# Kernel optimization log

Measured on AMD Instinct MI355X. Metric: run time of the kernel, lower is better.

Reference implementation:

```python
import jax, jax.numpy as jnp
import numpy as np

SEQ_LEN = 512
MAX_SPAN = 15
BATCH = 8
HIDDEN = 1024
WIDTH_DIM = 64
NUM_LABELS = 3


def _enumerate_spans(seq_len, max_span):
    starts, ends = [], []
    for s in range(seq_len):
        for e in range(s, min(s + max_span, seq_len)):
            starts.append(s)
            ends.append(e)
    return np.asarray(starts, np.int32), np.asarray(ends, np.int32)


def setup_inputs() -> dict:
    key = jax.random.key(0)
    k = jax.random.split(key, 6)
    starts, ends = _enumerate_spans(SEQ_LEN, MAX_SPAN)  # N = 7575
    d_in = HIDDEN * 2 + WIDTH_DIM  # 2112
    return {
        "sequence_output": jax.random.normal(k[0], (BATCH, SEQ_LEN, HIDDEN), jnp.float32),
        "width_emb": jax.random.normal(k[1], (MAX_SPAN, WIDTH_DIM), jnp.float32) * 0.02,
        "W1": jax.random.normal(k[2], (d_in, HIDDEN), jnp.float32) * (1.0 / np.sqrt(d_in)),
        "b1": jnp.zeros((HIDDEN,), jnp.float32),
        "W2": jax.random.normal(k[3], (HIDDEN, NUM_LABELS), jnp.float32) * (1.0 / np.sqrt(HIDDEN)),
        "b2": jnp.zeros((NUM_LABELS,), jnp.float32),
        "span_starts": jnp.asarray(starts),
        "span_ends": jnp.asarray(ends),
    }


def reference(sequence_output, width_emb, W1, b1, W2, b2, span_starts, span_ends):
    # Gather start/end token representations for every candidate span.
    B = sequence_output.shape[0]
    N = span_starts.shape[0]
    start_repr = sequence_output[:, span_starts]            # [B, N, H]
    end_repr = sequence_output[:, span_ends]                # [B, N, H]
    width_repr = width_emb[span_ends - span_starts]         # [N, 64]
    width_repr = jnp.broadcast_to(width_repr[None], (B, N, width_repr.shape[-1]))
    span_reprs = jnp.concatenate([start_repr, end_repr, width_repr], axis=-1)  # [B, N, 2H+64]
    # Span classifier MLP (dropout is identity in eval mode).
    h = jax.nn.relu(jnp.einsum("bnd,dh->bnh", span_reprs, W1) + b1)
    logits = jnp.einsum("bnh,hl->bnl", h, W2) + b2          # [B, N, num_labels]
    return logits
```

## Files before the change

### kernel.cpp

```cpp
#include <hip/hip_runtime.h>
#include <stdint.h>

#define SEQ 512
#define BATCH 8
#define HID 1024

typedef __attribute__((ext_vector_type(8))) __bf16 bf16x8;
typedef __attribute__((ext_vector_type(4))) float f32x4;

__device__ __forceinline__ unsigned short f2bf(float f) {
    unsigned int u = __float_as_uint(f);
    unsigned int r = 0x7fffu + ((u >> 16) & 1u);
    return (unsigned short)((u + r) >> 16);
}

__device__ __forceinline__ void unpack8(uint4 v, float* f) {
    f[0] = __uint_as_float(v.x << 16);
    f[1] = __uint_as_float(v.x & 0xffff0000u);
    f[2] = __uint_as_float(v.y << 16);
    f[3] = __uint_as_float(v.y & 0xffff0000u);
    f[4] = __uint_as_float(v.z << 16);
    f[5] = __uint_as_float(v.z & 0xffff0000u);
    f[6] = __uint_as_float(v.w << 16);
    f[7] = __uint_as_float(v.w & 0xffff0000u);
}

__global__ __launch_bounds__(256) void k_prep(const float* __restrict__ seq,
                                              const float* __restrict__ wemb,
                                              const float* __restrict__ W1,
                                              const float* __restrict__ b1,
                                              ushort* __restrict__ seqb,
                                              ushort* __restrict__ Bt,
                                              ushort* __restrict__ Rbf) {
    __shared__ float tile[32][33];
    const int bid = blockIdx.x;
    const int tid = threadIdx.x;
    if (bid < 4096) {
        int i = bid * 256 + tid;
        float4 v = ((const float4*)seq)[i];
        ushort4 o;
        o.x = f2bf(v.x); o.y = f2bf(v.y); o.z = f2bf(v.z); o.w = f2bf(v.w);
        ((ushort4*)seqb)[i] = o;
    } else if (bid < 6144) {
        int idx = bid - 4096;
        int nb = (idx & 63) * 32, kb = (idx >> 6) * 32;
        int tx = tid & 31, ty = tid >> 5;
        int n = nb + tx;
        int rb = (n < 1024) ? 0 : 1024;
        int nc = n - rb;
#pragma unroll
        for (int i = 0; i < 4; ++i) {
            int k = kb + ty + i * 8;
            tile[ty + i * 8][tx] = W1[(size_t)(rb + k) * 1024 + nc];
        }
        __syncthreads();
#pragma unroll
        for (int i = 0; i < 4; ++i) {
            int n2 = nb + ty + i * 8;
            Bt[(size_t)n2 * 1024 + kb + tx] = f2bf(tile[tx][ty + i * 8]);
        }
    } else {
        int idx = (bid - 6144) * 256 + tid;
        int w = idx >> 10, j = idx & 1023;
        float acc = b1[j];
#pragma unroll
        for (int c = 0; c < 64; ++c)
            acc = fmaf(wemb[w * 64 + c], W1[(size_t)(2048 + c) * 1024 + j], acc);
        Rbf[idx] = f2bf(acc);
    }
}

__global__ __launch_bounds__(512) void k_gemm(const ushort* __restrict__ A,
                                              const ushort* __restrict__ Bt,
                                              ushort* __restrict__ P,
                                              ushort* __restrict__ Q) {
    __shared__ ushort Al[2][8192];
    __shared__ ushort Bl[2][8192];
    const int tid = threadIdx.x;
    const int wid = tid >> 6;
    const int lane = tid & 63;
    const int bid = blockIdx.x;
    const int swz = ((bid & 7) << 6) | (bid >> 3);
    const int n0 = (swz & 15) * 128;
    const int m0 = (swz >> 4) * 128;
    const int wm = (wid >> 2) * 64;
    const int wn = (wid & 3) * 32;
    const int srow = lane >> 2;
    const int scol = (lane & 3) * 8;
    const int fr = lane & 15;
    const int fk = (lane >> 4) * 8;

    f32x4 acc[4][2] = {};

    const ushort* Abase = A  + (size_t)(m0 + srow) * 1024 + scol;
    const ushort* Bbase = Bt + (size_t)(n0 + srow) * 1024 + scol;

#define STAGE(buf, k0)                                                                     \
    {                                                                                      \
        _Pragma("unroll")                                                                  \
        for (int r = 0; r < 2; ++r) {                                                      \
            int c = wid + 8 * r;                                                           \
            int half = c >> 3;                                                             \
            int rows = (c & 7) * 16;                                                       \
            const ushort* sa = Abase + (size_t)rows * 1024 + (k0) + half * 32;             \
            const ushort* sb = Bbase + (size_t)rows * 1024 + (k0) + half * 32;             \
            int loff = half * 4096 + rows * 32;                                            \
            __builtin_amdgcn_global_load_lds((const __attribute__((address_space(1))) void*)sa, \
                                             (__attribute__((address_space(3))) void*)(&Al[buf][loff]), \
                                             16, 0, 0);                                    \
            __builtin_amdgcn_global_load_lds((const __attribute__((address_space(1))) void*)sb, \
                                             (__attribute__((address_space(3))) void*)(&Bl[buf][loff]), \
                                             16, 0, 0);                                    \
        }                                                                                  \
    }

    STAGE(0, 0);
    __syncthreads();

    for (int t = 0; t < 16; ++t) {
        const int cur = t & 1;
        if (t < 15) STAGE(cur ^ 1, (t + 1) * 64);
#pragma unroll
        for (int kk = 0; kk < 2; ++kk) {
            bf16x8 af[4], bg[2];
#pragma unroll
            for (int i = 0; i < 4; ++i)
                af[i] = *(const bf16x8*)(&Al[cur][kk * 4096 + (wm + i * 16 + fr) * 32 + fk]);
#pragma unroll
            for (int j = 0; j < 2; ++j)
                bg[j] = *(const bf16x8*)(&Bl[cur][kk * 4096 + (wn + j * 16 + fr) * 32 + fk]);
#pragma unroll
            for (int i = 0; i < 4; ++i)
#pragma unroll
                for (int j = 0; j < 2; ++j)
                    acc[i][j] = __builtin_amdgcn_mfma_f32_16x16x32_bf16(af[i], bg[j], acc[i][j], 0, 0, 0);
        }
        __syncthreads();
    }
#undef STAGE

    ushort* Cb = (n0 < 1024) ? P : Q;
    const int nc0 = n0 & 1023;
    const int cr = (lane >> 4) * 4;
    const int cc = lane & 15;
#pragma unroll
    for (int i = 0; i < 4; ++i)
#pragma unroll
        for (int j = 0; j < 2; ++j) {
            ushort* Cp = Cb + (size_t)(m0 + wm + i * 16 + cr) * 1024 + (nc0 + wn + j * 16 + cc);
#pragma unroll
            for (int r = 0; r < 4; ++r)
                Cp[(size_t)r * 1024] = f2bf(acc[i][j][r]);
        }
}

__global__ __launch_bounds__(1024) void k_span2(const ushort* __restrict__ Pmat,
                                                const ushort* __restrict__ Qmat,
                                                const ushort* __restrict__ Rbf,
                                                const float* __restrict__ W2,
                                                const float* __restrict__ b2,
                                                float* __restrict__ out, int nspans) {
    __shared__ ushort Qs[30 * 1024];
    __shared__ ushort Rs[15 * 1024];
    const int tid = threadIdx.x;
    const int wid = tid >> 6, lane = tid & 63;
    const int b = blockIdx.x >> 5;
    const int s0 = (blockIdx.x & 31) << 4;

#pragma unroll
    for (int i = 0; i < 4; ++i) {
        int c = wid + (i << 4);
        if (c < 60) {
            int g = (c << 9) + lane * 8;
            int row = s0 + (g >> 10);
            if (row > SEQ - 1) row = SEQ - 1;
            const ushort* src = Qmat + (((size_t)(b << 9) + row) << 10) + (g & 1023);
            __builtin_amdgcn_global_load_lds((const __attribute__((address_space(1))) void*)src,
                                             (__attribute__((address_space(3))) void*)(Qs + (c << 9)),
                                             16, 0, 0);
        }
    }
#pragma unroll
    for (int i = 0; i < 2; ++i) {
        int c = wid + (i << 4);
        if (c < 30) {
            int g = (c << 9) + lane * 8;
            __builtin_amdgcn_global_load_lds((const __attribute__((address_space(1))) void*)(Rbf + g),
                                             (__attribute__((address_space(3))) void*)(Rs + (c << 9)),
                                             16, 0, 0);
        }
    }

    float w2r[3][2][8];
#pragma unroll
    for (int it = 0; it < 2; ++it)
#pragma unroll
        for (int u = 0; u < 8; ++u) {
            int j = lane * 8 + it * 512 + u;
            w2r[0][it][u] = W2[j * 3 + 0];
            w2r[1][it][u] = W2[j * 3 + 1];
            w2r[2][it][u] = W2[j * 3 + 2];
        }
    const float bb0 = b2[0], bb1 = b2[1], bb2 = b2[2];

    const int s = s0 + wid;
    float pf[16];
    {
        const uint4* pr = (const uint4*)(Pmat + (((size_t)(b << 9) + s) << 10) + lane * 8);
        unpack8(pr[0], pf);
        unpack8(pr[64], pf + 8);
    }

    __syncthreads();

    const int rrem = SEQ - s;
    const int nsp = (rrem < 15) ? rrem : 15;
    const int off = (rrem >= 15) ? 15 * s : (7575 - (rrem * (rrem + 1)) / 2);
    float* op = out + ((size_t)b * nspans + off) * 3;

    for (int w = 0; w < nsp; ++w) {
        const int erow = wid + w;
        float a0 = 0.f, a1 = 0.f, a2 = 0.f;
#pragma unroll
        for (int it = 0; it < 2; ++it) {
            uint4 qv = *(const uint4*)((const char*)Qs + erow * 2048 + it * 1024 + lane * 16);
            uint4 rv = *(const uint4*)((const char*)Rs + w * 2048 + it * 1024 + lane * 16);
            float qf[8], rf[8];
            unpack8(qv, qf);
            unpack8(rv, rf);
#pragma unroll
            for (int u = 0; u < 8; ++u) {
                float h = pf[it * 8 + u] + qf[u] + rf[u];
                h = fmaxf(h, 0.f);
                a0 = fmaf(h, w2r[0][it][u], a0);
                a1 = fmaf(h, w2r[1][it][u], a1);
                a2 = fmaf(h, w2r[2][it][u], a2);
            }
        }
#pragma unroll
        for (int o = 32; o; o >>= 1) {
            a0 += __shfl_xor(a0, o);
            a1 += __shfl_xor(a1, o);
            a2 += __shfl_xor(a2, o);
        }
        if (lane == 0) {
            op[w * 3 + 0] = a0 + bb0;
            op[w * 3 + 1] = a1 + bb1;
            op[w * 3 + 2] = a2 + bb2;
        }
    }
}

extern "C" void kernel_launch(void* const* d_in, const int* in_sizes, int n_in,
                              void* d_out, int out_size, void* d_ws, size_t ws_size,
                              hipStream_t stream) {
    const float* seq    = (const float*)d_in[0];
    const float* wemb   = (const float*)d_in[1];
    const float* W1     = (const float*)d_in[2];
    const float* b1     = (const float*)d_in[3];
    const float* W2     = (const float*)d_in[4];
    const float* b2     = (const float*)d_in[5];
    float* out = (float*)d_out;
    int nspans = in_sizes[6];

    char* ws = (char*)d_ws;
    ushort* seqb = (ushort*)ws;
    ushort* Bt   = (ushort*)(ws + (8u << 20));
    ushort* Pmat = (ushort*)(ws + (12u << 20));
    ushort* Qmat = (ushort*)(ws + (20u << 20));
    ushort* Rbf  = (ushort*)(ws + (28u << 20));

    hipLaunchKernelGGL(k_prep, dim3(6204), dim3(256), 0, stream,
                       seq, wemb, W1, b1, seqb, Bt, Rbf);
    hipLaunchKernelGGL(k_gemm, dim3(512), dim3(512), 0, stream, seqb, Bt, Pmat, Qmat);
    hipLaunchKernelGGL(k_span2, dim3(BATCH * (SEQ / 16)), dim3(1024), 0, stream,
                       Pmat, Qmat, Rbf, W2, b2, out, nspans);
}
```

Baseline: 59.15 us.

## Pipeline GEMM loads with partial vmcnt waits, MFMA priority, and new tile swizzle

The GEMM main loop now waits only until the current stage's async global-to-LDS loads have landed (vmcnt(4)), so the next stage's prefetch stays in flight during compute. Raw barriers replace __syncthreads, and the last iteration is peeled. MFMA sections are wrapped in s_setprio to favour matrix issue, and the block-to-tile mapping is changed to group tiles per XCD for better L2 reuse. Relying on a hand-counted vmcnt is fragile if the compiler reorders or adds memory ops.

```diff
diff --git a/kernel.cpp b/kernel.cpp
--- a/kernel.cpp
+++ b/kernel.cpp
@@ -80,9 +80,9 @@
     const int wid = tid >> 6;
     const int lane = tid & 63;
     const int bid = blockIdx.x;
-    const int swz = ((bid & 7) << 6) | (bid >> 3);
-    const int n0 = (swz & 15) * 128;
-    const int m0 = (swz >> 4) * 128;
+    const int x = bid & 7, t8 = bid >> 3;
+    const int m0 = (((x >> 1) << 3) + (t8 >> 3)) * 128;
+    const int n0 = (((x & 1) << 3) + (t8 & 7)) * 128;
     const int wm = (wid >> 2) * 64;
     const int wn = (wid & 3) * 32;
     const int srow = lane >> 2;
@@ -114,30 +114,41 @@
         }                                                                                  \
     }
 
+#define COMPUTE(cur)                                                                       \
+    {                                                                                      \
+        _Pragma("unroll")                                                                  \
+        for (int kk = 0; kk < 2; ++kk) {                                                   \
+            bf16x8 af[4], bg[2];                                                           \
+            _Pragma("unroll")                                                              \
+            for (int i = 0; i < 4; ++i)                                                    \
+                af[i] = *(const bf16x8*)(&Al[cur][kk * 4096 + (wm + i * 16 + fr) * 32 + fk]); \
+            _Pragma("unroll")                                                              \
+            for (int j = 0; j < 2; ++j)                                                    \
+                bg[j] = *(const bf16x8*)(&Bl[cur][kk * 4096 + (wn + j * 16 + fr) * 32 + fk]); \
+            __builtin_amdgcn_s_setprio(1);                                                 \
+            _Pragma("unroll")                                                              \
+            for (int i = 0; i < 4; ++i)                                                    \
+                _Pragma("unroll")                                                          \
+                for (int j = 0; j < 2; ++j)                                                \
+                    acc[i][j] = __builtin_amdgcn_mfma_f32_16x16x32_bf16(af[i], bg[j], acc[i][j], 0, 0, 0); \
+            __builtin_amdgcn_s_setprio(0);                                                 \
+        }                                                                                  \
+    }
+
     STAGE(0, 0);
-    __syncthreads();
-
-    for (int t = 0; t < 16; ++t) {
+    for (int t = 0; t < 15; ++t) {
         const int cur = t & 1;
-        if (t < 15) STAGE(cur ^ 1, (t + 1) * 64);
-#pragma unroll
-        for (int kk = 0; kk < 2; ++kk) {
-            bf16x8 af[4], bg[2];
-#pragma unroll
-            for (int i = 0; i < 4; ++i)
-                af[i] = *(const bf16x8*)(&Al[cur][kk * 4096 + (wm + i * 16 + fr) * 32 + fk]);
-#pragma unroll
-            for (int j = 0; j < 2; ++j)
-                bg[j] = *(const bf16x8*)(&Bl[cur][kk * 4096 + (wn + j * 16 + fr) * 32 + fk]);
-#pragma unroll
-            for (int i = 0; i < 4; ++i)
-#pragma unroll
-                for (int j = 0; j < 2; ++j)
-                    acc[i][j] = __builtin_amdgcn_mfma_f32_16x16x32_bf16(af[i], bg[j], acc[i][j], 0, 0, 0);
-        }
-        __syncthreads();
-    }
+        STAGE(cur ^ 1, (t + 1) * 64);
+        asm volatile("s_waitcnt vmcnt(4)" ::: "memory");
+        __builtin_amdgcn_s_barrier();
+        COMPUTE(cur);
+        __builtin_amdgcn_s_barrier();
+    }
+    asm volatile("s_waitcnt vmcnt(0)" ::: "memory");
+    __builtin_amdgcn_s_barrier();
+    COMPUTE(1);
 #undef STAGE
+#undef COMPUTE
 
     ushort* Cb = (n0 < 1024) ? P : Q;
     const int nc0 = n0 & 1023;
```

Result: no change. 59.55 us (+0.7%).
